# Kernel tuning notes

Hardware: AMD Instinct MI355X
Metric: run time of the kernel (lower is better)

Reference implementation:

```python
import jax, jax.numpy as jnp
import numpy as np

TEMPERATURE = 0.1
NORMALIZE = True
EPS = 1e-8  # matches torch F.normalize eps-free clamp behavior closely enough for randn inputs

B, D = 4096, 512


def setup_inputs() -> dict:
    key = jax.random.key(0)
    k1, k2 = jax.random.split(key)
    z_i = jax.random.normal(k1, (B, D), dtype=jnp.float32)
    z_j = jax.random.normal(k2, (B, D), dtype=jnp.float32)
    return {"z_i": z_i, "z_j": z_j}


def _l2_normalize(x):
    # torch.F.normalize: x / max(||x||, eps)
    n = jnp.linalg.norm(x, axis=1, keepdims=True)
    return x / jnp.maximum(n, 1e-12)


def reference(z_i, z_j):
    b = z_i.shape[0]
    if NORMALIZE:
        z_i = _l2_normalize(z_i)
        z_j = _l2_normalize(z_j)
    z = jnp.concatenate([z_i, z_j], axis=0)               # (2B, D)
    logits = (z @ z.T) / TEMPERATURE                      # (2B, 2B)
    n = 2 * b
    diag = jnp.eye(n, dtype=bool)
    logits = jnp.where(diag, -jnp.inf, logits)
    row = jnp.arange(n)
    pos_col = (row + b) % n
    pos_logits = logits[row, pos_col]                     # (2B,)
    lse = jax.scipy.special.logsumexp(logits, axis=1)     # stable logsumexp per row
    loss = -(pos_logits - lse).mean()
    return loss
```

## Files before the change

kernel.cpp:

```cpp
#include <hip/hip_runtime.h>
#include <stdint.h>

#define D_DIM 512
#define B_ROWS 4096
#define N_ROWS 8192
#define SCALE_L2E 14.426950408889634f

#define NHP 8
#define NOFF (28 * 256)
#define NBLK (NOFF + 8 * 160)

typedef __attribute__((ext_vector_type(4))) float f32x4;
typedef __attribute__((ext_vector_type(2))) long f8x16;

__global__ __launch_bounds__(256) void k_normalize(const float* __restrict__ zi,
                                                   const float* __restrict__ zj,
                                                   unsigned char* __restrict__ Zn,
                                                   float* __restrict__ pos) {
    const int t = threadIdx.x;
    const int lane = t & 63;
    const int i = blockIdx.x * 4 + (t >> 6);
    const float* pa = zi + (size_t)i * D_DIM + lane * 8;
    const float* pb = zj + (size_t)i * D_DIM + lane * 8;
    const float4 a0 = *(const float4*)pa;
    const float4 a1 = *(const float4*)(pa + 4);
    const float4 b0 = *(const float4*)pb;
    const float4 b1 = *(const float4*)(pb + 4);
    float ssi = a0.x*a0.x + a0.y*a0.y + a0.z*a0.z + a0.w*a0.w
              + a1.x*a1.x + a1.y*a1.y + a1.z*a1.z + a1.w*a1.w;
    float ssj = b0.x*b0.x + b0.y*b0.y + b0.z*b0.z + b0.w*b0.w
              + b1.x*b1.x + b1.y*b1.y + b1.z*b1.z + b1.w*b1.w;
    float dt  = a0.x*b0.x + a0.y*b0.y + a0.z*b0.z + a0.w*b0.w
              + a1.x*b1.x + a1.y*b1.y + a1.z*b1.z + a1.w*b1.w;
    #pragma unroll
    for (int off = 1; off < 64; off <<= 1) {
        ssi += __shfl_xor(ssi, off);
        ssj += __shfl_xor(ssj, off);
        dt  += __shfl_xor(dt,  off);
    }
    const float si = 1.0f / fmaxf(sqrtf(ssi), 1e-12f);
    const float sj = 1.0f / fmaxf(sqrtf(ssj), 1e-12f);
    uint2 pi8, pj8;
    {
        int w0 = 0, w1 = 0;
        w0 = __builtin_amdgcn_cvt_pk_fp8_f32(a0.x * si, a0.y * si, w0, false);
        w0 = __builtin_amdgcn_cvt_pk_fp8_f32(a0.z * si, a0.w * si, w0, true);
        w1 = __builtin_amdgcn_cvt_pk_fp8_f32(a1.x * si, a1.y * si, w1, false);
        w1 = __builtin_amdgcn_cvt_pk_fp8_f32(a1.z * si, a1.w * si, w1, true);
        pi8.x = (unsigned)w0; pi8.y = (unsigned)w1;
        w0 = 0; w1 = 0;
        w0 = __builtin_amdgcn_cvt_pk_fp8_f32(b0.x * sj, b0.y * sj, w0, false);
        w0 = __builtin_amdgcn_cvt_pk_fp8_f32(b0.z * sj, b0.w * sj, w0, true);
        w1 = __builtin_amdgcn_cvt_pk_fp8_f32(b1.x * sj, b1.y * sj, w1, false);
        w1 = __builtin_amdgcn_cvt_pk_fp8_f32(b1.z * sj, b1.w * sj, w1, true);
        pj8.x = (unsigned)w0; pj8.y = (unsigned)w1;
    }
    const size_t PLANE = (size_t)N_ROWS * 64;
    const int o = lane & 7;
    const size_t off0 = (size_t)(lane >> 3) * PLANE + (o & 3) * 16 + (o >> 2) * 8;
    *(uint2*)(Zn + off0 + (size_t)i * 64) = pi8;
    *(uint2*)(Zn + off0 + (size_t)(B_ROWS + i) * 64) = pj8;
    if (lane == 0) pos[i] = 20.0f * dt * si * sj;
}

__global__ __launch_bounds__(64, 4) void k_gemm_lse(const unsigned char* __restrict__ Zn,
                                                    float* __restrict__ rowsum_g) {
    const int lane = threadIdx.x & 63;
    const int l15  = lane & 15, lhi = lane >> 4;

    const int s = (blockIdx.x & 7) * (NBLK / 8) + (blockIdx.x >> 3);
    int SI, SJ, di, dj;
    if (s < NOFF) {
        const int sp = s >> 8;
        int g = s & 255;
        int a = 0, b = 1;
        for (int k = 0; k < sp; ++k) { if (++b == 8) { ++a; b = a + 1; } }
        SI = a; SJ = b;
        const int q = g >> 5, r = g & 31;
        di = r & 15; dj = (r >> 4) * 8 + q;
    } else {
        int g = s - NOFF;
        const int S = g / 160;
        g = g % 160;
        if (g >= 136) return;
        SI = SJ = S;
        di = 0;
        while (g >= 16 - di) { g -= 16 - di; ++di; }
        dj = di + g;
    }
    const int I = SI * 16 + di, J = SJ * 16 + dj;
    const bool dg = (I == J);
    const int rowB = I * 64;
    const int colB = J * 64;

    const char* Zb = (const char*)Zn;
    const size_t PLANE = (size_t)N_ROWS * 64;

    const char* pA = Zb + ((size_t)(rowB + l15)) * 64 + lhi * 16;
    const char* pB = Zb + ((size_t)(colB + l15)) * 64 + lhi * 16;

    f32x4 acc[4][4];
    #pragma unroll
    for (int a = 0; a < 4; ++a)
        #pragma unroll
        for (int b = 0; b < 4; ++b)
            #pragma unroll
            for (int q = 0; q < 4; ++q) acc[a][b][q] = 0.0f;

    for (int hp = 0; hp < NHP; ++hp) {
        f8x16 af[4], bg[4];
        const char* _a = pA + (size_t)hp * PLANE;
        const char* _b = pB + (size_t)hp * PLANE;
        #pragma unroll
        for (int mi = 0; mi < 4; ++mi) af[mi] = *(const f8x16*)(_a + mi * 1024);
        #pragma unroll
        for (int ni = 0; ni < 4; ++ni) bg[ni] = *(const f8x16*)(_b + ni * 1024);
        __builtin_amdgcn_s_setprio(1);
        #pragma unroll
        for (int mi = 0; mi < 4; ++mi)
            #pragma unroll
            for (int ni = 0; ni < 4; ++ni)
                acc[mi][ni] = __builtin_amdgcn_mfma_f32_16x16x32_fp8_fp8(
                    af[mi][0], bg[ni][0], acc[mi][ni], 0, 0, 0);
        #pragma unroll
        for (int mi = 0; mi < 4; ++mi)
            #pragma unroll
            for (int ni = 0; ni < 4; ++ni)
                acc[mi][ni] = __builtin_amdgcn_mfma_f32_16x16x32_fp8_fp8(
                    af[mi][1], bg[ni][1], acc[mi][ni], 0, 0, 0);
        __builtin_amdgcn_s_setprio(0);
    }

    float colsum[4] = {0.0f, 0.0f, 0.0f, 0.0f};
    #pragma unroll
    for (int mi = 0; mi < 4; ++mi) {
        const int growb = rowB + mi * 16 + lhi * 4;
        float rs[4] = {0.0f, 0.0f, 0.0f, 0.0f};
        if (dg) {
            #pragma unroll
            for (int ni = 0; ni < 4; ++ni) {
                const int gcol = colB + ni * 16 + l15;
                #pragma unroll
                for (int r = 0; r < 4; ++r) {
                    float arg = acc[mi][ni][r] * SCALE_L2E;
                    if (growb + r == gcol) arg = -1e30f;
                    rs[r] += exp2f(arg);
                }
            }
        } else {
            #pragma unroll
            for (int ni = 0; ni < 4; ++ni)
                #pragma unroll
                for (int r = 0; r < 4; ++r) {
                    const float e = exp2f(acc[mi][ni][r] * SCALE_L2E);
                    rs[r] += e;
                    colsum[ni] += e;
                }
        }
        #pragma unroll
        for (int r = 0; r < 4; ++r) {
            float v = rs[r];
            v += __shfl_xor(v, 1);
            v += __shfl_xor(v, 2);
            v += __shfl_xor(v, 4);
            v += __shfl_xor(v, 8);
            if (l15 == 0) atomicAdd(&rowsum_g[growb + r], v);
        }
    }
    if (!dg) {
        #pragma unroll
        for (int ni = 0; ni < 4; ++ni) {
            float c = colsum[ni];
            c += __shfl_xor(c, 16);
            c += __shfl_xor(c, 32);
            if (lhi == 0)
                atomicAdd(&rowsum_g[colB + ni * 16 + l15], c);
        }
    }
}

__global__ __launch_bounds__(1024) void k_finalize(const float* __restrict__ rowsum_g,
                                                   const float* __restrict__ pos,
                                                   float* __restrict__ out) {
    const int t = threadIdx.x;
    float l = 0.0f, p = 0.0f;
    #pragma unroll
    for (int q = 0; q < N_ROWS / 1024; ++q) l += logf(rowsum_g[t + q * 1024]);
    #pragma unroll
    for (int q = 0; q < B_ROWS / 1024; ++q) p += pos[t + q * 1024];
    #pragma unroll
    for (int off = 1; off < 64; off <<= 1) {
        l += __shfl_xor(l, off);
        p += __shfl_xor(p, off);
    }
    __shared__ float red[2][16];
    if ((t & 63) == 0) { red[0][t >> 6] = l; red[1][t >> 6] = p; }
    __syncthreads();
    if (t == 0) {
        float L = 0.0f, P = 0.0f;
        #pragma unroll
        for (int q = 0; q < 16; ++q) { L += red[0][q]; P += red[1][q]; }
        out[0] = (L - P) * (1.0f / (float)N_ROWS);
    }
}

extern "C" void kernel_launch(void* const* d_in, const int* in_sizes, int n_in,
                              void* d_out, int out_size, void* d_ws, size_t ws_size,
                              hipStream_t stream) {
    (void)in_sizes; (void)n_in; (void)out_size; (void)ws_size;
    const float* zi = (const float*)d_in[0];
    const float* zj = (const float*)d_in[1];

    const size_t ZN_BYTES = (size_t)N_ROWS * D_DIM;
    unsigned char* Zn     = (unsigned char*)d_ws;
    float* rowsum_g       = (float*)((char*)d_ws + ZN_BYTES);
    float* pos            = (float*)((char*)d_ws + ZN_BYTES + N_ROWS * 4);

    hipMemsetAsync(rowsum_g, 0, N_ROWS * 4, stream);

    k_normalize<<<B_ROWS / 4, 256, 0, stream>>>(zi, zj, Zn, pos);
    k_gemm_lse<<<NBLK, 64, 0, stream>>>(Zn, rowsum_g);
    k_finalize<<<1, 1024, 0, stream>>>(rowsum_g, pos, (float*)d_out);
}
```

Baseline: 60.76 us.

## Triple-buffer fp8 GEMM K-stages, narrow plane layout, fuse rowsum zeroing into normalize

```diff
diff --git a/kernel.cpp b/kernel.cpp
--- a/kernel.cpp
+++ b/kernel.cpp
@@ -6,18 +6,23 @@
 #define N_ROWS 8192
 #define SCALE_L2E 14.426950408889634f
 
-#define NHP 8
+#define NST 16
 #define NOFF (28 * 256)
 #define NBLK (NOFF + 8 * 160)
 
 typedef __attribute__((ext_vector_type(4))) float f32x4;
-typedef __attribute__((ext_vector_type(2))) long f8x16;
+typedef long f8x8;
 
 __global__ __launch_bounds__(256) void k_normalize(const float* __restrict__ zi,
                                                    const float* __restrict__ zj,
                                                    unsigned char* __restrict__ Zn,
-                                                   float* __restrict__ pos) {
+                                                   float* __restrict__ pos,
+                                                   float* __restrict__ rowsum_g) {
     const int t = threadIdx.x;
+    if (blockIdx.x < 8) {
+        float4 z = {0.0f, 0.0f, 0.0f, 0.0f};
+        *(float4*)(rowsum_g + blockIdx.x * 1024 + t * 4) = z;
+    }
     const int lane = t & 63;
     const int i = blockIdx.x * 4 + (t >> 6);
     const float* pa = zi + (size_t)i * D_DIM + lane * 8;
@@ -55,11 +60,10 @@
         w1 = __builtin_amdgcn_cvt_pk_fp8_f32(b1.z * sj, b1.w * sj, w1, true);
         pj8.x = (unsigned)w0; pj8.y = (unsigned)w1;
     }
-    const size_t PLANE = (size_t)N_ROWS * 64;
-    const int o = lane & 7;
-    const size_t off0 = (size_t)(lane >> 3) * PLANE + (o & 3) * 16 + (o >> 2) * 8;
-    *(uint2*)(Zn + off0 + (size_t)i * 64) = pi8;
-    *(uint2*)(Zn + off0 + (size_t)(B_ROWS + i) * 64) = pj8;
+    const size_t PLANE = (size_t)N_ROWS * 32;
+    const size_t off0  = (size_t)(lane >> 2) * PLANE + (lane & 3) * 8;
+    *(uint2*)(Zn + off0 + (size_t)i * 32) = pi8;
+    *(uint2*)(Zn + off0 + (size_t)(B_ROWS + i) * 32) = pj8;
     if (lane == 0) pos[i] = 20.0f * dt * si * sj;
 }
 
@@ -94,10 +98,34 @@
     const int colB = J * 64;
 
     const char* Zb = (const char*)Zn;
-    const size_t PLANE = (size_t)N_ROWS * 64;
-
-    const char* pA = Zb + ((size_t)(rowB + l15)) * 64 + lhi * 16;
-    const char* pB = Zb + ((size_t)(colB + l15)) * 64 + lhi * 16;
+    const size_t PLANE = (size_t)N_ROWS * 32;
+
+    const char* pA = Zb + ((size_t)(rowB + l15)) * 32 + lhi * 8;
+    const char* pB = Zb + ((size_t)(colB + l15)) * 32 + lhi * 8;
+
+    f8x8 afa[4], bga[4], afb[4], bgb[4], afc[4], bgc[4];
+
+#define LOADAB(dstA, dstB, st)                                                     \
+    do {                                                                           \
+        const char* _a = pA + (size_t)(st) * PLANE;                                \
+        const char* _b = pB + (size_t)(st) * PLANE;                                \
+        _Pragma("unroll")                                                          \
+        for (int mi = 0; mi < 4; ++mi) dstA[mi] = *(const f8x8*)(_a + mi * 512);   \
+        _Pragma("unroll")                                                          \
+        for (int ni = 0; ni < 4; ++ni) dstB[ni] = *(const f8x8*)(_b + ni * 512);   \
+    } while (0)
+
+#define MFMAAB(srcA, srcB)                                                         \
+    do {                                                                           \
+        __builtin_amdgcn_s_setprio(1);                                             \
+        _Pragma("unroll")                                                          \
+        for (int mi = 0; mi < 4; ++mi)                                             \
+            _Pragma("unroll")                                                      \
+            for (int ni = 0; ni < 4; ++ni)                                         \
+                acc[mi][ni] = __builtin_amdgcn_mfma_f32_16x16x32_fp8_fp8(          \
+                    srcA[mi], srcB[ni], acc[mi][ni], 0, 0, 0);                     \
+        __builtin_amdgcn_s_setprio(0);                                             \
+    } while (0)
 
     f32x4 acc[4][4];
     #pragma unroll
@@ -107,28 +135,22 @@
             #pragma unroll
             for (int q = 0; q < 4; ++q) acc[a][b][q] = 0.0f;
 
-    for (int hp = 0; hp < NHP; ++hp) {
-        f8x16 af[4], bg[4];
-        const char* _a = pA + (size_t)hp * PLANE;
-        const char* _b = pB + (size_t)hp * PLANE;
-        #pragma unroll
-        for (int mi = 0; mi < 4; ++mi) af[mi] = *(const f8x16*)(_a + mi * 1024);
-        #pragma unroll
-        for (int ni = 0; ni < 4; ++ni) bg[ni] = *(const f8x16*)(_b + ni * 1024);
-        __builtin_amdgcn_s_setprio(1);
-        #pragma unroll
-        for (int mi = 0; mi < 4; ++mi)
-            #pragma unroll
-            for (int ni = 0; ni < 4; ++ni)
-                acc[mi][ni] = __builtin_amdgcn_mfma_f32_16x16x32_fp8_fp8(
-                    af[mi][0], bg[ni][0], acc[mi][ni], 0, 0, 0);
-        #pragma unroll
-        for (int mi = 0; mi < 4; ++mi)
-            #pragma unroll
-            for (int ni = 0; ni < 4; ++ni)
-                acc[mi][ni] = __builtin_amdgcn_mfma_f32_16x16x32_fp8_fp8(
-                    af[mi][1], bg[ni][1], acc[mi][ni], 0, 0, 0);
-        __builtin_amdgcn_s_setprio(0);
+    LOADAB(afa, bga, 0);
+    LOADAB(afb, bgb, 1);
+    LOADAB(afc, bgc, 2);
+
+    #pragma unroll
+    for (int st = 0; st < NST; ++st) {
+        if (st % 3 == 0) {
+            MFMAAB(afa, bga);
+            if (st + 3 < NST) LOADAB(afa, bga, st + 3);
+        } else if (st % 3 == 1) {
+            MFMAAB(afb, bgb);
+            if (st + 3 < NST) LOADAB(afb, bgb, st + 3);
+        } else {
+            MFMAAB(afc, bgc);
+            if (st + 3 < NST) LOADAB(afc, bgc, st + 3);
+        }
     }
 
     float colsum[4] = {0.0f, 0.0f, 0.0f, 0.0f};
@@ -177,6 +199,8 @@
                 atomicAdd(&rowsum_g[colB + ni * 16 + l15], c);
         }
     }
+#undef LOADAB
+#undef MFMAAB
 }
 
 __global__ __launch_bounds__(1024) void k_finalize(const float* __restrict__ rowsum_g,
@@ -216,9 +240,7 @@
     float* rowsum_g       = (float*)((char*)d_ws + ZN_BYTES);
     float* pos            = (float*)((char*)d_ws + ZN_BYTES + N_ROWS * 4);
 
-    hipMemsetAsync(rowsum_g, 0, N_ROWS * 4, stream);
-
-    k_normalize<<<B_ROWS / 4, 256, 0, stream>>>(zi, zj, Zn, pos);
+    k_normalize<<<B_ROWS / 4, 256, 0, stream>>>(zi, zj, Zn, pos, rowsum_g);
     k_gemm_lse<<<NBLK, 64, 0, stream>>>(Zn, rowsum_g);
     k_finalize<<<1, 1024, 0, stream>>>(rowsum_g, pos, (float*)d_out);
 }
```

After: 57.37 us (median of 2 runs). -5.6%, faster.
